# Optimization experiments

Hardware: AMD Instinct MI355X
Metric: run time of the kernel (lower is better)

The kernel has to match this reference:

```python
import jax, jax.numpy as jnp
import numpy as np

B, S, D = 8, 2048, 1024
NEG = jnp.float32(-(2.0**32) + 1.0)

def setup_inputs() -> dict:
    key = jax.random.key(0)
    ks = jax.random.split(key, 7)
    s = 1.0 / np.sqrt(D)
    return {
        "x": jax.random.normal(ks[0], (B, S, D), dtype=jnp.float32),
        "Wq": jax.random.normal(ks[1], (D, D), dtype=jnp.float32) * s,
        "bq": jnp.zeros((D,), dtype=jnp.float32),
        "Wk": jax.random.normal(ks[2], (D, D), dtype=jnp.float32) * s,
        "bk": jnp.zeros((D,), dtype=jnp.float32),
        "Wv": jax.random.normal(ks[3], (D, D), dtype=jnp.float32) * s,
        "bv": jnp.zeros((D,), dtype=jnp.float32),
    }

def reference(x, Wq, bq, Wk, bk, Wv, bv):
    # QKV projections with inline ReLU
    q = jax.nn.relu(jnp.einsum('bsd,df->bsf', x, Wq) + bq)
    k = jax.nn.relu(jnp.einsum('bsd,df->bsf', x, Wk) + bk)
    v = jax.nn.relu(jnp.einsum('bsd,df->bsf', x, Wv) + bv)
    # scaled scores [B, S, S]
    scores = jnp.einsum('bqd,bkd->bqk', q, k) / jnp.sqrt(jnp.float32(D))
    # sin-based key/query masks derived from token sums [B, S]
    masks = jnp.sin(jnp.abs(jnp.sum(x, axis=-1)))
    # mask keys where mask == 0
    scores = jnp.where(masks[:, None, :] == 0, NEG, scores)
    attn = jax.nn.softmax(scores, axis=-1)
    # post-softmax query masking (broadcast over keys)
    attn = attn * masks[:, :, None]
    out = jnp.einsum('bqk,bkd->bqd', attn, v) + q  # residual add of q
    return out
```

## Files before the change

### kernel.cpp

```cpp
#include <hip/hip_runtime.h>

#define DEV __device__ __forceinline__

typedef __attribute__((ext_vector_type(8))) short bf16x8;
typedef __attribute__((ext_vector_type(4))) float f32x4;

static constexpr int Bn = 8;
static constexpr int Sn = 2048;
static constexpr int Dn = 1024;
static constexpr int Mtot = Bn * Sn;

static constexpr int ABUF = 8192;
static constexpr int TBUF = 12288;
static constexpr int BUFS_A = 16384;
static constexpr int BHALF_A = 8192;

DEV void gload_lds16(const void* g, void* l) {
  __builtin_amdgcn_global_load_lds(
      (const __attribute__((address_space(1))) void*)g,
      (__attribute__((address_space(3))) void*)l, 16, 0, 0);
}

DEV float bf2f(unsigned short u) {
  union { unsigned int i; float f; } c;
  c.i = ((unsigned int)u) << 16;
  return c.f;
}
DEV unsigned short f2bf(float f) {
  union { float f; unsigned int i; } c;
  c.f = f;
  unsigned int lsb = (c.i >> 16) & 1u;
  return (unsigned short)((c.i + 0x7fffu + lsb) >> 16);
}

__global__ __launch_bounds__(256) void prep_kernel(const float* __restrict__ x,
                                                   unsigned short* __restrict__ xbf,
                                                   float* __restrict__ masks) {
  const int w = threadIdx.x >> 6, l = threadIdx.x & 63;
  const int row = blockIdx.x * 4 + w;
  const float* xr = x + (size_t)row * Dn;
  unsigned short* xo = xbf + (size_t)row * Dn;
  float s = 0.f;
  #pragma unroll
  for (int i = 0; i < 4; i++) {
    float4 v = ((const float4*)xr)[i * 64 + l];
    s += (v.x + v.y) + (v.z + v.w);
    unsigned int p0 = (unsigned int)f2bf(v.x) | ((unsigned int)f2bf(v.y) << 16);
    unsigned int p1 = (unsigned int)f2bf(v.z) | ((unsigned int)f2bf(v.w) << 16);
    *(uint2*)&xo[i * 256 + l * 4] = make_uint2(p0, p1);
  }
  #pragma unroll
  for (int off = 32; off > 0; off >>= 1) s += __shfl_xor(s, off);
  if (l == 0) masks[row] = sinf(fabsf(s));
}

__global__ __launch_bounds__(256) void wt_kernel(const float* __restrict__ Wq,
                                                 const float* __restrict__ Wk,
                                                 const float* __restrict__ Wv,
                                                 unsigned short* __restrict__ Wt) {
  const float* W = blockIdx.z == 0 ? Wq : (blockIdx.z == 1 ? Wk : Wv);
  unsigned short* out = Wt + (size_t)blockIdx.z * Dn * Dn;
  __shared__ float tile[32][33];
  const int r0 = blockIdx.y * 32, c0 = blockIdx.x * 32;
  const int t = threadIdx.x;
  {
    const int r = t >> 3, c4 = (t & 7) * 4;
    float4 v = *(const float4*)&W[(size_t)(r0 + r) * Dn + c0 + c4];
    tile[r][c4 + 0] = v.x; tile[r][c4 + 1] = v.y;
    tile[r][c4 + 2] = v.z; tile[r][c4 + 3] = v.w;
  }
  __syncthreads();
  {
    const int f = t >> 3, d4 = (t & 7) * 4;
    unsigned short o[4];
    #pragma unroll
    for (int i = 0; i < 4; i++) o[i] = f2bf(tile[d4 + i][f]);
    unsigned int p0 = (unsigned int)o[0] | ((unsigned int)o[1] << 16);
    unsigned int p1 = (unsigned int)o[2] | ((unsigned int)o[3] << 16);
    *(uint2*)&out[(size_t)(c0 + f) * Dn + r0 + d4] = make_uint2(p0, p1);
  }
}

DEV void gemmB(const unsigned short* __restrict__ Ag, int lda,
               const unsigned short* __restrict__ Bg, int ldb,
               int K, unsigned short* lds, f32x4 acc[4][4]) {
  const int tid = threadIdx.x;
  const int l = tid & 63, w = tid >> 6;
  const int wr = w >> 1, wc = w & 1;
  const int lr = l & 15, lk = l >> 4;

  #pragma unroll
  for (int mi = 0; mi < 4; mi++)
    #pragma unroll
    for (int ni = 0; ni < 4; ni++)
      #pragma unroll
      for (int q = 0; q < 4; q++) acc[mi][ni][q] = 0.f;

  int offA[4], offB[4];
  #pragma unroll
  for (int mi = 0; mi < 4; mi++) {
    const int row = wr * 64 + mi * 16 + lr;
    offA[mi] = (row * 4 + (lk ^ ((row >> 1) & 3))) * 8;
  }
  #pragma unroll
  for (int ni = 0; ni < 4; ni++) {
    const int row = wc * 64 + ni * 16 + lr;
    offB[ni] = (row * 4 + (lk ^ ((row >> 1) & 3))) * 8;
  }
  int sA[2], dA[2], sB, dB;
  #pragma unroll
  for (int i = 0; i < 2; i++) {
    const int ci = i * 512 + tid;
    const int row = ci >> 2, c = (ci & 3) ^ ((row >> 1) & 3);
    sA[i] = row * lda + c * 8;
    dA[i] = ci * 8;
  }
  {
    const int ci = tid;
    const int row = ci >> 2, c = (ci & 3) ^ ((row >> 1) & 3);
    sB = row * ldb + c * 8;
    dB = ci * 8;
  }

  const int NT = K >> 5;
  unsigned short* bc = lds;
  unsigned short* b1 = lds + TBUF;
  unsigned short* b2 = lds + 2 * TBUF;

  #pragma unroll
  for (int t = 0; t < 2; t++) {
    unsigned short* bf = lds + t * TBUF;
    gload_lds16(Ag + sA[0] + t * 32, bf + dA[0]);
    gload_lds16(Ag + sA[1] + t * 32, bf + dA[1]);
    gload_lds16(Bg + sB + t * 32, bf + ABUF + dB);
  }
  asm volatile("s_waitcnt vmcnt(3)\n\ts_barrier" ::: "memory");

  for (int t = 0; t < NT; t++) {
    const bool st = (t + 2 < NT);
    const int kt = (t + 2) * 32;

    bf16x8 af[4], bv[4];
    #pragma unroll
    for (int mi = 0; mi < 4; mi++) af[mi] = *(const bf16x8*)(bc + offA[mi]);
    #pragma unroll
    for (int ni = 0; ni < 4; ni++) bv[ni] = *(const bf16x8*)(bc + ABUF + offB[ni]);

    if (st) {
      gload_lds16(Ag + sA[0] + kt, b2 + dA[0]);
      gload_lds16(Ag + sA[1] + kt, b2 + dA[1]);
    }
    __builtin_amdgcn_s_setprio(1);
    #pragma unroll
    for (int mi = 0; mi < 4; mi++) {
      acc[mi][0] = __builtin_amdgcn_mfma_f32_16x16x32_bf16(af[mi], bv[0], acc[mi][0], 0, 0, 0);
      acc[mi][1] = __builtin_amdgcn_mfma_f32_16x16x32_bf16(af[mi], bv[1], acc[mi][1], 0, 0, 0);
    }
    __builtin_amdgcn_s_setprio(0);
    if (st) {
      gload_lds16(Bg + sB + kt, b2 + ABUF + dB);
    }
    __builtin_amdgcn_s_setprio(1);
    #pragma unroll
    for (int mi = 0; mi < 4; mi++) {
      acc[mi][2] = __builtin_amdgcn_mfma_f32_16x16x32_bf16(af[mi], bv[2], acc[mi][2], 0, 0, 0);
      acc[mi][3] = __builtin_amdgcn_mfma_f32_16x16x32_bf16(af[mi], bv[3], acc[mi][3], 0, 0, 0);
    }
    __builtin_amdgcn_s_setprio(0);

    if (t + 2 < NT) {
      asm volatile("s_waitcnt vmcnt(3)\n\ts_barrier" ::: "memory");
    } else if (t + 1 < NT) {
      asm volatile("s_waitcnt vmcnt(0)\n\ts_barrier" ::: "memory");
    }
    unsigned short* tmp = bc; bc = b1; b1 = b2; b2 = tmp;
  }
}

DEV void gemmA(const unsigned short* __restrict__ Ag, int lda,
               const unsigned short* __restrict__ Bg, int ldb,
               int K, unsigned short* lds, f32x4 acc[8][4]) {
  const int tid = threadIdx.x;
  const int l = tid & 63, w = tid >> 6;
  const int wr = w >> 2, wc = w & 3;
  const int lr = l & 15, lk = l >> 4;

  #pragma unroll
  for (int mi = 0; mi < 8; mi++)
    #pragma unroll
    for (int ni = 0; ni < 4; ni++)
      #pragma unroll
      for (int q = 0; q < 4; q++) acc[mi][ni][q] = 0.f;

  int offA[8], offB[4];
  #pragma unroll
  for (int mi = 0; mi < 8; mi++) {
    const int row = wr * 128 + mi * 16 + lr;
    const int L = row >> 1, p = ((row & 1) * 4 + lk) ^ (L & 7);
    offA[mi] = L * 64 + p * 8;
  }
  #pragma unroll
  for (int ni = 0; ni < 4; ni++) {
    const int row = wc * 64 + ni * 16 + lr;
    const int L = row >> 1, p = ((row & 1) * 4 + lk) ^ (L & 7);
    offB[ni] = L * 64 + p * 8;
  }
  int sA[2], sB[2], dO[2];
  #pragma unroll
  for (int i = 0; i < 2; i++) {
    const int ci = i * 512 + tid;
    const int L = ci >> 3, p = ci & 7, e = p ^ (L & 7);
    const int grow = 2 * L + (e >> 2), gkc = e & 3;
    sA[i] = grow * lda + gkc * 8;
    sB[i] = grow * ldb + gkc * 8;
    dO[i] = ci * 8;
  }

  const int NT = K >> 5;
  #pragma unroll
  for (int t = 0; t < 3; t++) {
    unsigned short* bf = lds + t * BUFS_A;
    gload_lds16(Ag + sA[0] + t * 32, bf + dO[0]);
    gload_lds16(Ag + sA[1] + t * 32, bf + dO[1]);
    gload_lds16(Bg + sB[0] + t * 32, bf + BHALF_A + dO[0]);
    gload_lds16(Bg + sB[1] + t * 32, bf + BHALF_A + dO[1]);
  }
  asm volatile("s_waitcnt vmcnt(8)\n\ts_barrier" ::: "memory");

  for (int t = 0; t < NT; t++) {
    unsigned short* bufc = lds + (t & 3) * BUFS_A;
    unsigned short* bufs = lds + ((t + 3) & 3) * BUFS_A;
    const bool st = (t + 3 < NT);
    const int kt = (t + 3) * 32;

    bf16x8 af[8], bv[4];
    #pragma unroll
    for (int mi = 0; mi < 8; mi++) af[mi] = *(const bf16x8*)(bufc + offA[mi]);
    bv[0] = *(const bf16x8*)(bufc + BHALF_A + offB[0]);
    bv[1] = *(const bf16x8*)(bufc + BHALF_A + offB[1]);
    if (st) {
      gload_lds16(Ag + sA[0] + kt, bufs + dO[0]);
      gload_lds16(Ag + sA[1] + kt, bufs + dO[1]);
    }
    __builtin_amdgcn_s_setprio(1);
    #pragma unroll
    for (int mi = 0; mi < 8; mi++) {
      acc[mi][0] = __builtin_amdgcn_mfma_f32_16x16x32_bf16(af[mi], bv[0], acc[mi][0], 0, 0, 0);
      acc[mi][1] = __builtin_amdgcn_mfma_f32_16x16x32_bf16(af[mi], bv[1], acc[mi][1], 0, 0, 0);
    }
    __builtin_amdgcn_s_setprio(0);
    bv[2] = *(const bf16x8*)(bufc + BHALF_A + offB[2]);
    bv[3] = *(const bf16x8*)(bufc + BHALF_A + offB[3]);
    if (st) {
      gload_lds16(Bg + sB[0] + kt, bufs + BHALF_A + dO[0]);
      gload_lds16(Bg + sB[1] + kt, bufs + BHALF_A + dO[1]);
    }
    __builtin_amdgcn_s_setprio(1);
    #pragma unroll
    for (int mi = 0; mi < 8; mi++) {
      acc[mi][2] = __builtin_amdgcn_mfma_f32_16x16x32_bf16(af[mi], bv[2], acc[mi][2], 0, 0, 0);
      acc[mi][3] = __builtin_amdgcn_mfma_f32_16x16x32_bf16(af[mi], bv[3], acc[mi][3], 0, 0, 0);
    }
    __builtin_amdgcn_s_setprio(0);

    if (t < NT - 3) {
      asm volatile("s_waitcnt vmcnt(8)\n\ts_barrier" ::: "memory");
    } else if (t == NT - 3) {
      asm volatile("s_waitcnt vmcnt(4)\n\ts_barrier" ::: "memory");
    } else if (t == NT - 2) {
      asm volatile("s_waitcnt vmcnt(0)\n\ts_barrier" ::: "memory");
    }
  }
}

__global__ __launch_bounds__(512, 4) void qkv_kernel(
    const unsigned short* __restrict__ xbf, const unsigned short* __restrict__ Wt,
    const float* __restrict__ bq, const float* __restrict__ bk,
    const float* __restrict__ bv_,
    unsigned short* __restrict__ qo, unsigned short* __restrict__ ko,
    unsigned short* __restrict__ vT) {
  __shared__ __align__(16) unsigned short lds[3 * TBUF];
  const int orig = blockIdx.x;
  const int wg = (orig & 7) * 192 + (orig >> 3);
  const int which = wg >> 9;
  const int rem = wg & 511;
  const int m0 = (rem >> 3) * 256, n0 = (rem & 7) * 128;
  const unsigned short* Ag = xbf + (size_t)m0 * Dn;
  const unsigned short* Bg = Wt + (size_t)which * Dn * Dn + (size_t)n0 * Dn;
  f32x4 acc[4][4];
  gemmB(Ag, Dn, Bg, Dn, Dn, lds, acc);

  const float* bias = which == 0 ? bq : (which == 1 ? bk : bv_);
  const int tid = threadIdx.x;
  const int l = tid & 63, w = tid >> 6;
  const int wr = w >> 1, wc = w & 1;
  const int lr = l & 15, lk = l >> 4;

  if (which < 2) {
    unsigned short* out = which == 0 ? qo : ko;
    #pragma unroll
    for (int mi = 0; mi < 4; mi++) {
      #pragma unroll
      for (int ni = 0; ni < 4; ni++) {
        const int col = n0 + wc * 64 + ni * 16 + lr;
        const float bcol = bias[col];
        #pragma unroll
        for (int j = 0; j < 4; j++) {
          const int row = m0 + wr * 64 + mi * 16 + lk * 4 + j;
          out[(size_t)row * Dn + col] = f2bf(fmaxf(acc[mi][ni][j] + bcol, 0.f));
        }
      }
    }
  } else {
    const int b = m0 >> 11;
    const int s0g = m0 & (Sn - 1);
    __syncthreads();
    #pragma unroll
    for (int mi = 0; mi < 4; mi++) {
      const int sc = wr * 16 + mi * 4 + lk;
      #pragma unroll
      for (int ni = 0; ni < 4; ni++) {
        const int d = wc * 64 + ni * 16 + lr;
        const float bcol = bias[n0 + d];
        unsigned short o0 = f2bf(fmaxf(acc[mi][ni][0] + bcol, 0.f));
        unsigned short o1 = f2bf(fmaxf(acc[mi][ni][1] + bcol, 0.f));
        unsigned short o2 = f2bf(fmaxf(acc[mi][ni][2] + bcol, 0.f));
        unsigned short o3 = f2bf(fmaxf(acc[mi][ni][3] + bcol, 0.f));
        const int scp = sc ^ (d & 63);
        *(uint2*)&lds[d * 256 + scp * 4] =
            make_uint2((unsigned int)o0 | ((unsigned int)o1 << 16),
                       (unsigned int)o2 | ((unsigned int)o3 << 16));
      }
    }
    __syncthreads();
    #pragma unroll
    for (int it = 0; it < 16; it++) {
      const int lin = it * 512 + tid;
      const int d = lin >> 6, sc = lin & 63;
      const int scp = sc ^ (d & 63);
      uint2 v = *(const uint2*)&lds[d * 256 + scp * 4];
      *(uint2*)&vT[((size_t)b * Dn + n0 + d) * Sn + s0g + sc * 4] = v;
    }
  }
}

__global__ __launch_bounds__(512, 2) void scores_kernel(
    const unsigned short* __restrict__ qbf, const unsigned short* __restrict__ kbf,
    const float* __restrict__ masks, unsigned short* __restrict__ P,
    float* __restrict__ lpart) {
  __shared__ __align__(16) unsigned short lds[4 * BUFS_A];
  const int orig = blockIdx.x;
  const int wg = (orig & 7) * 64 + (orig >> 3);
  const int b = wg >> 6;
  const int rem = wg & 63;
  const int m0 = (rem >> 3) * 256, n0 = (rem & 7) * 256;
  const unsigned short* Ag = qbf + ((size_t)b * Sn + m0) * Dn;
  const unsigned short* Bg = kbf + ((size_t)b * Sn + n0) * Dn;
  f32x4 acc[8][4];
  gemmA(Ag, Dn, Bg, Dn, Dn, lds, acc);

  const int tid = threadIdx.x;
  const int l = tid & 63, w = tid >> 6;
  const int wr = w >> 2, wc = w & 3;
  const int lr = l & 15, lk = l >> 4;

  __syncthreads();
  float* psum = (float*)lds;

  float mkv[4];
  #pragma unroll
  for (int ni = 0; ni < 4; ni++) mkv[ni] = masks[b * Sn + n0 + wc * 64 + ni * 16 + lr];

  unsigned short* Pb = P + (size_t)b * Sn * Sn;
  #pragma unroll
  for (int mi = 0; mi < 8; mi++) {
    #pragma unroll
    for (int j = 0; j < 4; j++) {
      const int rloc = wr * 128 + mi * 16 + lk * 4 + j;
      const size_t rbase = (size_t)(m0 + rloc) * Sn;
      float rsum = 0.f;
      #pragma unroll
      for (int ni = 0; ni < 4; ni++) {
        const int col = n0 + wc * 64 + ni * 16 + lr;
        const float p = (mkv[ni] == 0.f) ? 0.f : __expf(acc[mi][ni][j] * 0.03125f);
        const unsigned short pq = f2bf(p);
        Pb[rbase + col] = pq;
        rsum += bf2f(pq);
      }
      rsum += __shfl_xor(rsum, 1); rsum += __shfl_xor(rsum, 2);
      rsum += __shfl_xor(rsum, 4); rsum += __shfl_xor(rsum, 8);
      if (lr == 0) psum[wc * 256 + rloc] = rsum;
    }
  }
  __syncthreads();
  if (tid < 256) {
    const float v = psum[tid] + psum[256 + tid] + psum[512 + tid] + psum[768 + tid];
    lpart[((size_t)b * Sn + m0 + tid) * 8 + (rem & 7)] = v;
  }
}

__global__ __launch_bounds__(512, 2) void pv_kernel(
    const unsigned short* __restrict__ P, const unsigned short* __restrict__ vT,
    const float* __restrict__ lpart, const float* __restrict__ masks,
    const unsigned short* __restrict__ qbf, float* __restrict__ out) {
  __shared__ __align__(16) unsigned short lds[4 * BUFS_A];
  const int orig = blockIdx.x;
  const int wg = (orig & 7) * 32 + (orig >> 3);
  const int b = wg >> 5;
  const int rem = wg & 31;
  const int m0 = (rem >> 2) * 256, n0 = (rem & 3) * 256;
  const unsigned short* Ag = P + (size_t)b * Sn * Sn + (size_t)m0 * Sn;
  const unsigned short* Bg = vT + (size_t)b * Dn * Sn + (size_t)n0 * Sn;
  f32x4 acc[8][4];
  gemmA(Ag, Sn, Bg, Sn, Sn, lds, acc);

  const int tid = threadIdx.x;
  const int l = tid & 63, w = tid >> 6;
  const int wr = w >> 2, wc = w & 3;
  const int lr = l & 15, lk = l >> 4;

  __syncthreads();
  float* lsc = (float*)lds;
  if (tid < 256) {
    const float4* p4 = (const float4*)(lpart + ((size_t)b * Sn + m0 + tid) * 8);
    float4 a4 = p4[0], b4 = p4[1];
    const float sum = ((a4.x + a4.y) + (a4.z + a4.w)) + ((b4.x + b4.y) + (b4.z + b4.w));
    lsc[tid] = masks[b * Sn + m0 + tid] / sum;
  }
  __syncthreads();

  #pragma unroll
  for (int mi = 0; mi < 8; mi++) {
    #pragma unroll
    for (int j = 0; j < 4; j++) {
      const int rloc = wr * 128 + mi * 16 + lk * 4 + j;
      const float sc = lsc[rloc];
      const size_t rbase = ((size_t)b * Sn + m0 + rloc) * Dn;
      #pragma unroll
      for (int ni = 0; ni < 4; ni++) {
        const int col = n0 + wc * 64 + ni * 16 + lr;
        out[rbase + col] = acc[mi][ni][j] * sc + bf2f(qbf[rbase + col]);
      }
    }
  }
}

extern "C" void kernel_launch(void* const* d_in, const int* in_sizes, int n_in,
                              void* d_out, int out_size, void* d_ws, size_t ws_size,
                              hipStream_t stream) {
  const float* x  = (const float*)d_in[0];
  const float* Wq = (const float*)d_in[1];
  const float* bq = (const float*)d_in[2];
  const float* Wk = (const float*)d_in[3];
  const float* bk = (const float*)d_in[4];
  const float* Wv = (const float*)d_in[5];
  const float* bv = (const float*)d_in[6];
  float* out = (float*)d_out;

  char* ws = (char*)d_ws;
  size_t off = 0;
  auto alloc = [&](size_t bytes) {
    char* p = ws + off;
    off += (bytes + 255) & ~(size_t)255;
    return p;
  };
  unsigned short* xbf = (unsigned short*)alloc((size_t)Mtot * Dn * 2);
  unsigned short* qbf = (unsigned short*)alloc((size_t)Mtot * Dn * 2);
  unsigned short* kbf = (unsigned short*)alloc((size_t)Mtot * Dn * 2);
  unsigned short* vT  = (unsigned short*)alloc((size_t)Bn * Dn * Sn * 2);
  unsigned short* P   = (unsigned short*)alloc((size_t)Bn * Sn * Sn * 2);
  unsigned short* Wt  = (unsigned short*)alloc((size_t)3 * Dn * Dn * 2);
  float* masks = (float*)alloc((size_t)Mtot * 4);
  float* lpart = (float*)alloc((size_t)Mtot * 8 * 4);

  prep_kernel<<<Mtot / 4, 256, 0, stream>>>(x, xbf, masks);
  wt_kernel<<<dim3(32, 32, 3), 256, 0, stream>>>(Wq, Wk, Wv, Wt);
  qkv_kernel<<<1536, 512, 0, stream>>>(xbf, Wt, bq, bk, bv, qbf, kbf, vT);
  scores_kernel<<<512, 512, 0, stream>>>(qbf, kbf, masks, P, lpart);
  pv_kernel<<<256, 512, 0, stream>>>(P, vT, lpart, masks, qbf, out);
}
```

Before: 274.4 us.

## Process two adjacent output tiles per workgroup with continuous pipeline across tiles

Adds dual-tile GEMM variants that compute two consecutive N-tiles per workgroup, sharing the A-row tile and keeping the global-to-LDS prefetch pipeline running across the tile boundary, with an epilogue callback fired mid-loop. The QK projection and the scores kernel now launch half as many workgroups (256 and 512 instead of 512 and 1536 combined), aiming to cut pipeline fill and drain and per-block launch overhead. The V projection is split into its own kernel, launched after scores. The mid-loop epilogue adds barriers and stores while prefetches are in flight, and fewer workgroups may leave CUs underused.

```diff
diff --git a/kernel.cpp b/kernel.cpp
--- a/kernel.cpp
+++ b/kernel.cpp
@@ -81,6 +81,116 @@
   }
 }
 
+template <typename EPI>
+DEV void gemmB_dual(const unsigned short* __restrict__ Ag, int lda,
+                    const unsigned short* __restrict__ Bg0,
+                    const unsigned short* __restrict__ Bg1, int ldb,
+                    unsigned short* lds, f32x4 (&acc)[4][4], EPI epi) {
+  const int tid = threadIdx.x;
+  const int l = tid & 63, w = tid >> 6;
+  const int wr = w >> 1, wc = w & 1;
+  const int lr = l & 15, lk = l >> 4;
+
+  #pragma unroll
+  for (int mi = 0; mi < 4; mi++)
+    #pragma unroll
+    for (int ni = 0; ni < 4; ni++)
+      #pragma unroll
+      for (int q = 0; q < 4; q++) acc[mi][ni][q] = 0.f;
+
+  int offA[4], offB[4];
+  #pragma unroll
+  for (int mi = 0; mi < 4; mi++) {
+    const int row = wr * 64 + mi * 16 + lr;
+    offA[mi] = (row * 4 + (lk ^ ((row >> 1) & 3))) * 8;
+  }
+  #pragma unroll
+  for (int ni = 0; ni < 4; ni++) {
+    const int row = wc * 64 + ni * 16 + lr;
+    offB[ni] = (row * 4 + (lk ^ ((row >> 1) & 3))) * 8;
+  }
+  int sA[2], dA[2], sB, dB;
+  #pragma unroll
+  for (int i = 0; i < 2; i++) {
+    const int ci = i * 512 + tid;
+    const int row = ci >> 2, c = (ci & 3) ^ ((row >> 1) & 3);
+    sA[i] = row * lda + c * 8;
+    dA[i] = ci * 8;
+  }
+  {
+    const int ci = tid;
+    const int row = ci >> 2, c = (ci & 3) ^ ((row >> 1) & 3);
+    sB = row * ldb + c * 8;
+    dB = ci * 8;
+  }
+
+  const int NT = 32, G = 64;
+  auto bsrc = [&](int g) {
+    return (g >= NT) ? Bg1 + (size_t)(g - NT) * 32 : Bg0 + (size_t)g * 32;
+  };
+  auto akt = [&](int g) { return (g >= NT ? g - NT : g) * 32; };
+
+  #pragma unroll
+  for (int t = 0; t < 2; t++) {
+    unsigned short* bf = lds + t * TBUF;
+    gload_lds16(Ag + sA[0] + akt(t), bf + dA[0]);
+    gload_lds16(Ag + sA[1] + akt(t), bf + dA[1]);
+    gload_lds16(bsrc(t) + sB, bf + ABUF + dB);
+  }
+  asm volatile("s_waitcnt vmcnt(3)\n\ts_barrier" ::: "memory");
+
+  for (int g = 0; g < G; g++) {
+    unsigned short* bc = lds + (g % 3) * TBUF;
+    unsigned short* b2 = lds + ((g + 2) % 3) * TBUF;
+    const bool st = (g + 2 < G);
+
+    bf16x8 af[4], bv[4];
+    #pragma unroll
+    for (int mi = 0; mi < 4; mi++) af[mi] = *(const bf16x8*)(bc + offA[mi]);
+    #pragma unroll
+    for (int ni = 0; ni < 4; ni++) bv[ni] = *(const bf16x8*)(bc + ABUF + offB[ni]);
+
+    if (st) {
+      const int kt = akt(g + 2);
+      gload_lds16(Ag + sA[0] + kt, b2 + dA[0]);
+      gload_lds16(Ag + sA[1] + kt, b2 + dA[1]);
+    }
+    __builtin_amdgcn_s_setprio(1);
+    #pragma unroll
+    for (int mi = 0; mi < 4; mi++) {
+      acc[mi][0] = __builtin_amdgcn_mfma_f32_16x16x32_bf16(af[mi], bv[0], acc[mi][0], 0, 0, 0);
+      acc[mi][1] = __builtin_amdgcn_mfma_f32_16x16x32_bf16(af[mi], bv[1], acc[mi][1], 0, 0, 0);
+    }
+    __builtin_amdgcn_s_setprio(0);
+    if (st) {
+      gload_lds16(bsrc(g + 2) + sB, b2 + ABUF + dB);
+    }
+    __builtin_amdgcn_s_setprio(1);
+    #pragma unroll
+    for (int mi = 0; mi < 4; mi++) {
+      acc[mi][2] = __builtin_amdgcn_mfma_f32_16x16x32_bf16(af[mi], bv[2], acc[mi][2], 0, 0, 0);
+      acc[mi][3] = __builtin_amdgcn_mfma_f32_16x16x32_bf16(af[mi], bv[3], acc[mi][3], 0, 0, 0);
+    }
+    __builtin_amdgcn_s_setprio(0);
+
+    if (g + 2 < G) {
+      asm volatile("s_waitcnt vmcnt(3)\n\ts_barrier" ::: "memory");
+    } else if (g + 1 < G) {
+      asm volatile("s_waitcnt vmcnt(0)\n\ts_barrier" ::: "memory");
+    }
+    if (g == NT - 1) {
+      epi(0);
+      #pragma unroll
+      for (int mi = 0; mi < 4; mi++)
+        #pragma unroll
+        for (int ni = 0; ni < 4; ni++)
+          #pragma unroll
+          for (int q = 0; q < 4; q++) acc[mi][ni][q] = 0.f;
+    }
+  }
+  epi(1);
+}
+
 DEV void gemmB(const unsigned short* __restrict__ Ag, int lda,
                const unsigned short* __restrict__ Bg, int ldb,
                int K, unsigned short* lds, f32x4 acc[4][4]) {
@@ -177,6 +287,119 @@
   }
 }
 
+template <typename EPI>
+DEV void gemmA_dual(const unsigned short* __restrict__ Ag, int lda,
+                    const unsigned short* __restrict__ Bg0,
+                    const unsigned short* __restrict__ Bg1, int ldb,
+                    unsigned short* lds, f32x4 (&acc)[8][4], EPI epi) {
+  const int tid = threadIdx.x;
+  const int l = tid & 63, w = tid >> 6;
+  const int wr = w >> 2, wc = w & 3;
+  const int lr = l & 15, lk = l >> 4;
+
+  #pragma unroll
+  for (int mi = 0; mi < 8; mi++)
+    #pragma unroll
+    for (int ni = 0; ni < 4; ni++)
+      #pragma unroll
+      for (int q = 0; q < 4; q++) acc[mi][ni][q] = 0.f;
+
+  int offA[8], offB[4];
+  #pragma unroll
+  for (int mi = 0; mi < 8; mi++) {
+    const int row = wr * 128 + mi * 16 + lr;
+    const int L = row >> 1, p = ((row & 1) * 4 + lk) ^ (L & 7);
+    offA[mi] = L * 64 + p * 8;
+  }
+  #pragma unroll
+  for (int ni = 0; ni < 4; ni++) {
+    const int row = wc * 64 + ni * 16 + lr;
+    const int L = row >> 1, p = ((row & 1) * 4 + lk) ^ (L & 7);
+    offB[ni] = L * 64 + p * 8;
+  }
+  int sA[2], sB[2], dO[2];
+  #pragma unroll
+  for (int i = 0; i < 2; i++) {
+    const int ci = i * 512 + tid;
+    const int L = ci >> 3, p = ci & 7, e = p ^ (L & 7);
+    const int grow = 2 * L + (e >> 2), gkc = e & 3;
+    sA[i] = grow * lda + gkc * 8;
+    sB[i] = grow * ldb + gkc * 8;
+    dO[i] = ci * 8;
+  }
+
+  const int NT = 32, G = 64;
+  auto bsrc = [&](int g) {
+    return (g >= NT) ? Bg1 + (size_t)(g - NT) * 32 : Bg0 + (size_t)g * 32;
+  };
+  auto akt = [&](int g) { return (g >= NT ? g - NT : g) * 32; };
+
+  #pragma unroll
+  for (int t = 0; t < 3; t++) {
+    unsigned short* bf = lds + t * BUFS_A;
+    gload_lds16(Ag + sA[0] + akt(t), bf + dO[0]);
+    gload_lds16(Ag + sA[1] + akt(t), bf + dO[1]);
+    gload_lds16(bsrc(t) + sB[0], bf + BHALF_A + dO[0]);
+    gload_lds16(bsrc(t) + sB[1], bf + BHALF_A + dO[1]);
+  }
+  asm volatile("s_waitcnt vmcnt(8)\n\ts_barrier" ::: "memory");
+
+  for (int g = 0; g < G; g++) {
+    unsigned short* bufc = lds + (g & 3) * BUFS_A;
+    unsigned short* bufs = lds + ((g + 3) & 3) * BUFS_A;
+    const bool st = (g + 3 < G);
+    const int kt = akt(g + 3);
+
+    bf16x8 af[8], bv[4];
+    #pragma unroll
+    for (int mi = 0; mi < 8; mi++) af[mi] = *(const bf16x8*)(bufc + offA[mi]);
+    bv[0] = *(const bf16x8*)(bufc + BHALF_A + offB[0]);
+    bv[1] = *(const bf16x8*)(bufc + BHALF_A + offB[1]);
+    if (st) {
+      gload_lds16(Ag + sA[0] + kt, bufs + dO[0]);
+      gload_lds16(Ag + sA[1] + kt, bufs + dO[1]);
+    }
+    __builtin_amdgcn_s_setprio(1);
+    #pragma unroll
+    for (int mi = 0; mi < 8; mi++) {
+      acc[mi][0] = __builtin_amdgcn_mfma_f32_16x16x32_bf16(af[mi], bv[0], acc[mi][0], 0, 0, 0);
+      acc[mi][1] = __builtin_amdgcn_mfma_f32_16x16x32_bf16(af[mi], bv[1], acc[mi][1], 0, 0, 0);
+    }
+    __builtin_amdgcn_s_setprio(0);
+    bv[2] = *(const bf16x8*)(bufc + BHALF_A + offB[2]);
+    bv[3] = *(const bf16x8*)(bufc + BHALF_A + offB[3]);
+    if (st) {
+      gload_lds16(bsrc(g + 3) + sB[0], bufs + BHALF_A + dO[0]);
+      gload_lds16(bsrc(g + 3) + sB[1], bufs + BHALF_A + dO[1]);
+    }
+    __builtin_amdgcn_s_setprio(1);
+    #pragma unroll
+    for (int mi = 0; mi < 8; mi++) {
+      acc[mi][2] = __builtin_amdgcn_mfma_f32_16x16x32_bf16(af[mi], bv[2], acc[mi][2], 0, 0, 0);
+      acc[mi][3] = __builtin_amdgcn_mfma_f32_16x16x32_bf16(af[mi], bv[3], acc[mi][3], 0, 0, 0);
+    }
+    __builtin_amdgcn_s_setprio(0);
+
+    if (g < G - 3) {
+      asm volatile("s_waitcnt vmcnt(8)\n\ts_barrier" ::: "memory");
+    } else if (g == G - 3) {
+      asm volatile("s_waitcnt vmcnt(4)\n\ts_barrier" ::: "memory");
+    } else if (g == G - 2) {
+      asm volatile("s_waitcnt vmcnt(0)\n\ts_barrier" ::: "memory");
+    }
+    if (g == NT - 1) {
+      epi(0);
+      #pragma unroll
+      for (int mi = 0; mi < 8; mi++)
+        #pragma unroll
+        for (int ni = 0; ni < 4; ni++)
+          #pragma unroll
+          for (int q = 0; q < 4; q++) acc[mi][ni][q] = 0.f;
+    }
+  }
+  epi(1);
+}
+
 DEV void gemmA(const unsigned short* __restrict__ Ag, int lda,
                const unsigned short* __restrict__ Bg, int ldb,
                int K, unsigned short* lds, f32x4 acc[8][4]) {
@@ -273,36 +496,35 @@
   }
 }
 
-__global__ __launch_bounds__(512, 4) void qkv_kernel(
+__global__ __launch_bounds__(512, 4) void qk_kernel(
     const unsigned short* __restrict__ xbf, const unsigned short* __restrict__ Wt,
     const float* __restrict__ bq, const float* __restrict__ bk,
-    const float* __restrict__ bv_,
-    unsigned short* __restrict__ qo, unsigned short* __restrict__ ko,
-    unsigned short* __restrict__ vT) {
+    unsigned short* __restrict__ qo, unsigned short* __restrict__ ko) {
   __shared__ __align__(16) unsigned short lds[3 * TBUF];
   const int orig = blockIdx.x;
-  const int wg = (orig & 7) * 192 + (orig >> 3);
-  const int which = wg >> 9;
-  const int rem = wg & 511;
-  const int m0 = (rem >> 3) * 256, n0 = (rem & 7) * 128;
+  const int wg = (orig & 7) * 64 + (orig >> 3);
+  const int which = wg >> 8;
+  const int rem = wg & 255;
+  const int m0 = (rem >> 2) * 256, n0 = (rem & 3) * 256;
   const unsigned short* Ag = xbf + (size_t)m0 * Dn;
-  const unsigned short* Bg = Wt + (size_t)which * Dn * Dn + (size_t)n0 * Dn;
-  f32x4 acc[4][4];
-  gemmB(Ag, Dn, Bg, Dn, Dn, lds, acc);
-
-  const float* bias = which == 0 ? bq : (which == 1 ? bk : bv_);
+  const unsigned short* Bg0 = Wt + (size_t)which * Dn * Dn + (size_t)n0 * Dn;
+  const unsigned short* Bg1 = Bg0 + (size_t)128 * Dn;
+
+  const float* bias = which == 0 ? bq : bk;
+  unsigned short* out = which == 0 ? qo : ko;
   const int tid = threadIdx.x;
   const int l = tid & 63, w = tid >> 6;
   const int wr = w >> 1, wc = w & 1;
   const int lr = l & 15, lk = l >> 4;
 
-  if (which < 2) {
-    unsigned short* out = which == 0 ? qo : ko;
+  f32x4 acc[4][4];
+  gemmB_dual(Ag, Dn, Bg0, Bg1, Dn, lds, acc, [&](int tt) {
+    const int nb = n0 + tt * 128;
     #pragma unroll
     for (int mi = 0; mi < 4; mi++) {
       #pragma unroll
       for (int ni = 0; ni < 4; ni++) {
-        const int col = n0 + wc * 64 + ni * 16 + lr;
+        const int col = nb + wc * 64 + ni * 16 + lr;
         const float bcol = bias[col];
         #pragma unroll
         for (int j = 0; j < 4; j++) {
@@ -311,36 +533,54 @@
         }
       }
     }
-  } else {
-    const int b = m0 >> 11;
-    const int s0g = m0 & (Sn - 1);
-    __syncthreads();
-    #pragma unroll
-    for (int mi = 0; mi < 4; mi++) {
-      const int sc = wr * 16 + mi * 4 + lk;
-      #pragma unroll
-      for (int ni = 0; ni < 4; ni++) {
-        const int d = wc * 64 + ni * 16 + lr;
-        const float bcol = bias[n0 + d];
-        unsigned short o0 = f2bf(fmaxf(acc[mi][ni][0] + bcol, 0.f));
-        unsigned short o1 = f2bf(fmaxf(acc[mi][ni][1] + bcol, 0.f));
-        unsigned short o2 = f2bf(fmaxf(acc[mi][ni][2] + bcol, 0.f));
-        unsigned short o3 = f2bf(fmaxf(acc[mi][ni][3] + bcol, 0.f));
-        const int scp = sc ^ (d & 63);
-        *(uint2*)&lds[d * 256 + scp * 4] =
-            make_uint2((unsigned int)o0 | ((unsigned int)o1 << 16),
-                       (unsigned int)o2 | ((unsigned int)o3 << 16));
-      }
-    }
-    __syncthreads();
-    #pragma unroll
-    for (int it = 0; it < 16; it++) {
-      const int lin = it * 512 + tid;
-      const int d = lin >> 6, sc = lin & 63;
+  });
+}
+
+__global__ __launch_bounds__(512, 4) void v_kernel(
+    const unsigned short* __restrict__ xbf, const unsigned short* __restrict__ Wt,
+    const float* __restrict__ bv_, unsigned short* __restrict__ vT) {
+  __shared__ __align__(16) unsigned short lds[3 * TBUF];
+  const int orig = blockIdx.x;
+  const int wg = (orig & 7) * 64 + (orig >> 3);
+  const int m0 = (wg >> 3) * 256, n0 = (wg & 7) * 128;
+  const unsigned short* Ag = xbf + (size_t)m0 * Dn;
+  const unsigned short* Bg = Wt + (size_t)2 * Dn * Dn + (size_t)n0 * Dn;
+  f32x4 acc[4][4];
+  gemmB(Ag, Dn, Bg, Dn, Dn, lds, acc);
+
+  const int tid = threadIdx.x;
+  const int l = tid & 63, w = tid >> 6;
+  const int wr = w >> 1, wc = w & 1;
+  const int lr = l & 15, lk = l >> 4;
+
+  const int b = m0 >> 11;
+  const int s0g = m0 & (Sn - 1);
+  __syncthreads();
+  #pragma unroll
+  for (int mi = 0; mi < 4; mi++) {
+    const int sc = wr * 16 + mi * 4 + lk;
+    #pragma unroll
+    for (int ni = 0; ni < 4; ni++) {
+      const int d = wc * 64 + ni * 16 + lr;
+      const float bcol = bv_[n0 + d];
+      unsigned short o0 = f2bf(fmaxf(acc[mi][ni][0] + bcol, 0.f));
+      unsigned short o1 = f2bf(fmaxf(acc[mi][ni][1] + bcol, 0.f));
+      unsigned short o2 = f2bf(fmaxf(acc[mi][ni][2] + bcol, 0.f));
+      unsigned short o3 = f2bf(fmaxf(acc[mi][ni][3] + bcol, 0.f));
       const int scp = sc ^ (d & 63);
-      uint2 v = *(const uint2*)&lds[d * 256 + scp * 4];
-      *(uint2*)&vT[((size_t)b * Dn + n0 + d) * Sn + s0g + sc * 4] = v;
-    }
+      *(uint2*)&lds[d * 256 + scp * 4] =
+          make_uint2((unsigned int)o0 | ((unsigned int)o1 << 16),
+                     (unsigned int)o2 | ((unsigned int)o3 << 16));
+    }
+  }
+  __syncthreads();
+  #pragma unroll
+  for (int it = 0; it < 16; it++) {
+    const int lin = it * 512 + tid;
+    const int d = lin >> 6, sc = lin & 63;
+    const int scp = sc ^ (d & 63);
+    uint2 v = *(const uint2*)&lds[d * 256 + scp * 4];
+    *(uint2*)&vT[((size_t)b * Dn + n0 + d) * Sn + s0g + sc * 4] = v;
   }
 }
 
@@ -348,55 +588,57 @@
     const unsigned short* __restrict__ qbf, const unsigned short* __restrict__ kbf,
     const float* __restrict__ masks, unsigned short* __restrict__ P,
     float* __restrict__ lpart) {
-  __shared__ __align__(16) unsigned short lds[4 * BUFS_A];
+  __shared__ __align__(16) unsigned short lds[4 * BUFS_A + 2048];
   const int orig = blockIdx.x;
-  const int wg = (orig & 7) * 64 + (orig >> 3);
-  const int b = wg >> 6;
-  const int rem = wg & 63;
-  const int m0 = (rem >> 3) * 256, n0 = (rem & 7) * 256;
+  const int wg = (orig & 7) * 32 + (orig >> 3);
+  const int b = wg >> 5;
+  const int rem = wg & 31;
+  const int m0 = (rem >> 2) * 256, n0 = (rem & 3) * 512;
   const unsigned short* Ag = qbf + ((size_t)b * Sn + m0) * Dn;
-  const unsigned short* Bg = kbf + ((size_t)b * Sn + n0) * Dn;
-  f32x4 acc[8][4];
-  gemmA(Ag, Dn, Bg, Dn, Dn, lds, acc);
+  const unsigned short* Bg0 = kbf + ((size_t)b * Sn + n0) * Dn;
+  const unsigned short* Bg1 = Bg0 + (size_t)256 * Dn;
 
   const int tid = threadIdx.x;
   const int l = tid & 63, w = tid >> 6;
   const int wr = w >> 2, wc = w & 3;
   const int lr = l & 15, lk = l >> 4;
-
-  __syncthreads();
-  float* psum = (float*)lds;
-
-  float mkv[4];
-  #pragma unroll
-  for (int ni = 0; ni < 4; ni++) mkv[ni] = masks[b * Sn + n0 + wc * 64 + ni * 16 + lr];
-
+  float* psum = (float*)(lds + 4 * BUFS_A);
   unsigned short* Pb = P + (size_t)b * Sn * Sn;
-  #pragma unroll
-  for (int mi = 0; mi < 8; mi++) {
-    #pragma unroll
-    for (int j = 0; j < 4; j++) {
-      const int rloc = wr * 128 + mi * 16 + lk * 4 + j;
-      const size_t rbase = (size_t)(m0 + rloc) * Sn;
-      float rsum = 0.f;
-      #pragma unroll
-      for (int ni = 0; ni < 4; ni++) {
-        const int col = n0 + wc * 64 + ni * 16 + lr;
-        const float p = (mkv[ni] == 0.f) ? 0.f : __expf(acc[mi][ni][j] * 0.03125f);
-        const unsigned short pq = f2bf(p);
-        Pb[rbase + col] = pq;
-        rsum += bf2f(pq);
+
+  f32x4 acc[8][4];
+  gemmA_dual(Ag, Dn, Bg0, Bg1, Dn, lds, acc, [&](int tt) {
+    const int nb = n0 + tt * 256;
+    float mkv[4];
+    #pragma unroll
+    for (int ni = 0; ni < 4; ni++)
+      mkv[ni] = masks[b * Sn + nb + wc * 64 + ni * 16 + lr];
+    __syncthreads();
+    #pragma unroll
+    for (int mi = 0; mi < 8; mi++) {
+      #pragma unroll
+      for (int j = 0; j < 4; j++) {
+        const int rloc = wr * 128 + mi * 16 + lk * 4 + j;
+        const size_t rbase = (size_t)(m0 + rloc) * Sn;
+        float rsum = 0.f;
+        #pragma unroll
+        for (int ni = 0; ni < 4; ni++) {
+          const int col = nb + wc * 64 + ni * 16 + lr;
+          const float p = (mkv[ni] == 0.f) ? 0.f : __expf(acc[mi][ni][j] * 0.03125f);
+          const unsigned short pq = f2bf(p);
+          Pb[rbase + col] = pq;
+          rsum += bf2f(pq);
+        }
+        rsum += __shfl_xor(rsum, 1); rsum += __shfl_xor(rsum, 2);
+        rsum += __shfl_xor(rsum, 4); rsum += __shfl_xor(rsum, 8);
+        if (lr == 0) psum[wc * 256 + rloc] = rsum;
       }
-      rsum += __shfl_xor(rsum, 1); rsum += __shfl_xor(rsum, 2);
-      rsum += __shfl_xor(rsum, 4); rsum += __shfl_xor(rsum, 8);
-      if (lr == 0) psum[wc * 256 + rloc] = rsum;
-    }
-  }
-  __syncthreads();
-  if (tid < 256) {
-    const float v = psum[tid] + psum[256 + tid] + psum[512 + tid] + psum[768 + tid];
-    lpart[((size_t)b * Sn + m0 + tid) * 8 + (rem & 7)] = v;
-  }
+    }
+    __syncthreads();
+    if (tid < 256) {
+      const float v = psum[tid] + psum[256 + tid] + psum[512 + tid] + psum[768 + tid];
+      lpart[((size_t)b * Sn + m0 + tid) * 8 + ((rem & 3) * 2 + tt)] = v;
+    }
+  });
 }
 
 __global__ __launch_bounds__(512, 2) void pv_kernel(
@@ -475,7 +717,8 @@
 
   prep_kernel<<<Mtot / 4, 256, 0, stream>>>(x, xbf, masks);
   wt_kernel<<<dim3(32, 32, 3), 256, 0, stream>>>(Wq, Wk, Wv, Wt);
-  qkv_kernel<<<1536, 512, 0, stream>>>(xbf, Wt, bq, bk, bv, qbf, kbf, vT);
-  scores_kernel<<<512, 512, 0, stream>>>(qbf, kbf, masks, P, lpart);
+  qk_kernel<<<512, 512, 0, stream>>>(xbf, Wt, bq, bk, qbf, kbf);
+  scores_kernel<<<256, 512, 0, stream>>>(qbf, kbf, masks, P, lpart);
+  v_kernel<<<512, 512, 0, stream>>>(xbf, Wt, bv, vT);
   pv_kernel<<<256, 512, 0, stream>>>(P, vT, lpart, masks, qbf, out);
 }
```

New measurement: 404.0 us. +47.2%, slower.
